# Optimization experiments

Hardware: AMD Instinct MI355X
Metric: run time of the kernel (lower is better)

The kernel has to match this reference:

```python
import jax, jax.numpy as jnp
import numpy as np

ZERO = 1e-8
L = 2            # num_gnn_layers
D = 256          # dim_node_features
B = 32           # graphs per batch
NPG = 256        # nodes per graph
N = B * NPG      # total nodes
E = 131072       # edges per edge-type
MAX_TOKENS = 256 # MAX_TOKENS_OF_A_POST
UPD = 0.5        # args.updated_weights_for_A


def _make_edges(k):
    k1, k2, k3 = jax.random.split(k, 3)
    g = jax.random.randint(k1, (E,), 0, B) * NPG          # keep edges within a graph
    src = g + jax.random.randint(k2, (E,), 0, NPG)
    dst = g + jax.random.randint(k3, (E,), 0, NPG)
    return jnp.stack([src, dst]).astype(jnp.int64)


def setup_inputs() -> dict:
    key = jax.random.key(0)
    ks = jax.random.split(key, 12)
    x = jax.random.normal(ks[0], (N, D), dtype=jnp.float32)
    ei_e = _make_edges(ks[1]); ew_e = jax.random.uniform(ks[2], (E,), dtype=jnp.float32)
    ei_p = _make_edges(ks[3]); ew_p = jax.random.uniform(ks[4], (E,), dtype=jnp.float32)
    ei_o = _make_edges(ks[5]); ew_o = jax.random.uniform(ks[6], (E,), dtype=jnp.float32)
    entity_mask = jax.random.randint(ks[7], (B, NPG), 0, 2).astype(bool)
    pattern_mask = jax.random.randint(ks[8], (B, NPG), 0, 2).astype(bool)
    s = 1.0 / np.sqrt(D)
    W_gcn = (jax.random.normal(ks[9], (L, 3, D, D), dtype=jnp.float32) * s)
    b_gcn = jnp.zeros((L, 3, D), dtype=jnp.float32)
    T_dyn = (jax.random.normal(ks[10], (L, D, D), dtype=jnp.float32) * s)
    return {
        'x': x,
        'edge_index_entity': ei_e, 'edge_weight_entity': ew_e,
        'edge_index_pattern': ei_p, 'edge_weight_pattern': ew_p,
        'edge_index_others': ei_o, 'edge_weight_others': ew_o,
        'entity_mask': entity_mask, 'pattern_mask': pattern_mask,
        'W_gcn': W_gcn, 'b_gcn': b_gcn, 'T_dyn': T_dyn,
    }


def _normalized_correlation_matrix(H):
    # cosine-similarity correlation matrix, symmetrically degree-normalized
    nrm = jnp.sqrt(jnp.sum(H * H, axis=1))
    A = (H @ H.T) / (nrm[:, None] * nrm[None, :] + ZERO)
    dinv = 1.0 / jnp.sqrt(jnp.abs(jnp.sum(A, axis=1)) + ZERO)
    return dinv[:, None] * A * dinv[None, :]


def _gcn(H, W, b, ei, ew):
    # GCNConv(add_self_loops=False, normalize=False): scatter-sum of weighted source messages
    msg = (H @ W)[ei[0]] * ew[:, None]                     # [E, D]
    return jax.ops.segment_sum(msg, ei[1], num_segments=N) + b


def _forward(x, we0, wp0, wo0, W_gcn, b_gcn, T_dyn,
             ei_e, ei_p, ei_o, entity_mask, pattern_mask):
    H = x
    A = _normalized_correlation_matrix(H)                  # [N, N]
    for i in range(L):
        if i == 0:
            we, wp, wo = we0, wp0, wo0
        else:
            # diag(one_hot(src) @ A @ one_hot(dst).T) == A[src, dst]
            we = A[ei_e[0], ei_e[1]]
            wp = A[ei_p[0], ei_p[1]]
            wo = A[ei_o[0], ei_o[1]]
        He = _gcn(H, W_gcn[i, 0], b_gcn[i, 0], ei_e, we)
        Hp = _gcn(H, W_gcn[i, 1], b_gcn[i, 1], ei_p, wp)
        Ho = _gcn(H, W_gcn[i, 2], b_gcn[i, 2], ei_o, wo)
        H = jax.nn.relu(He + Hp + Ho)
        A_hat = jax.nn.sigmoid((H @ T_dyn[i]) @ H.T)
        A = (1.0 - UPD) * A + UPD * A_hat
    # per-graph diagonal blocks of A  -> [B, NPG, NPG]
    A4 = A.reshape(B, NPG, B, NPG)
    idx = jnp.arange(B)
    blocks = A4[idx, :, idx, :]
    A_sum = jnp.sum(blocks, axis=-1)                       # [B, NPG]
    ent_cols = jnp.einsum('bij,bj->bi', blocks, entity_mask.astype(A.dtype))
    pat_cols = jnp.einsum('bij,bj->bi', blocks, pattern_mask.astype(A.dtype))
    map_pattern = A_sum - ent_cols
    map_entity = A_sum - pat_cols

    def finish(m):
        mn = jnp.min(m, axis=1, keepdims=True)
        mx = jnp.max(m, axis=1, keepdims=True)
        m = (m - mn) / (mx - mn + ZERO)
        m = m / (jnp.sum(m, axis=1, keepdims=True) + ZERO)
        return m[:, :MAX_TOKENS]                           # padding() with NPG==MAX_TOKENS

    return finish(map_entity), finish(map_pattern)


def reference(x, edge_index_entity, edge_weight_entity,
              edge_index_pattern, edge_weight_pattern,
              edge_index_others, edge_weight_others,
              entity_mask, pattern_mask, W_gcn, b_gcn, T_dyn):
    return _forward(x, edge_weight_entity, edge_weight_pattern, edge_weight_others,
                    W_gcn, b_gcn, T_dyn,
                    edge_index_entity, edge_index_pattern, edge_index_others,
                    entity_mask, pattern_mask)
```

## Files before the change

### kernel.cpp

```cpp
#include <hip/hip_runtime.h>

#define NND   8192
#define DDIM  256
#define NGRP  32
#define ZEROF 1e-8f
#define KSTR  72
#define TSTR  72
#define CCAP 192
#define SM_HALF 36864
#define SM_FULL 55296

typedef unsigned short u16;
typedef __attribute__((ext_vector_type(8))) short short8v;
typedef __attribute__((ext_vector_type(4))) float float4v;

__device__ inline u16 f2bf(float x) {
  unsigned u = __float_as_uint(x);
  u += 0x7fffu + ((u >> 16) & 1u);
  return (u16)(u >> 16);
}
__device__ inline float bf2f(u16 h) { return __uint_as_float((unsigned)h << 16); }
__device__ inline void split2(float x, u16& h, u16& l) {
  h = f2bf(x);
  l = f2bf(x - bf2f(h));
}

__device__ inline float wave_sum(float v) {
#pragma unroll
  for (int off = 32; off > 0; off >>= 1) v += __shfl_down(v, off, 64);
  return v;
}

#define LOAD_REGS(tt, kk)                                                                   \
  {                                                                                         \
    int m_ = tid >> 2, kq_ = (tid & 3) * 8;                                                 \
    size_t aoff_;                                                                           \
    if (MODE == 1)                                                                          \
      aoff_ = (size_t)((tt) * 256 + bym * 64 + m_) * 8192 + (size_t)(g * 256 + (kk) + kq_); \
    else if (MODE == 2 || MODE == 3 || MODE == 5)                                           \
      aoff_ = (size_t)(g * 256 + bym * 64 + m_) * 256 + (kk) + kq_;                         \
    else                                                                                    \
      aoff_ = (size_t)(bym * 64 + m_) * 256 + (kk) + kq_;                                   \
    rA[0][0] = *(const short8v*)&Ah_g[aoff_];                                               \
    rA[0][1] = *(const short8v*)&Ah_g[aoff_ + 32];                                          \
    rA[1][0] = *(const short8v*)&Al_g[aoff_];                                               \
    rA[1][1] = *(const short8v*)&Al_g[aoff_ + 32];                                          \
    size_t bbase_ = (MODE == 1) ? ((size_t)(g * 3 + (tt)) << 16)                            \
                  : ((MODE == 2 || MODE == 3 || MODE == 5) ? ((size_t)g << 16) : (size_t)0);\
    if (HALF) {                                                                             \
      int n_ = tid & 63, kq2_ = (tid >> 6) * 8;                                             \
      size_t boff_ = bbase_ + (size_t)(col0 + n_) * 256 + (kk) + kq2_;                      \
      rB[0][0] = *(const short8v*)&Bh_g[boff_];                                             \
      rB[0][1] = *(const short8v*)&Bh_g[boff_ + 32];                                        \
      rB[1][0] = *(const short8v*)&Bl_g[boff_];                                             \
      rB[1][1] = *(const short8v*)&Bl_g[boff_ + 32];                                        \
    } else {                                                                                \
      int n_ = tid & 127, kq2_ = (tid >> 7) * 16;                                           \
      size_t boff_ = bbase_ + (size_t)(col0 + n_) * 256 + (kk) + kq2_;                      \
      rB[0][0] = *(const short8v*)&Bh_g[boff_];     rB[0][1] = *(const short8v*)&Bh_g[boff_ + 8];  \
      rB[0][2] = *(const short8v*)&Bh_g[boff_ + 32]; rB[0][3] = *(const short8v*)&Bh_g[boff_ + 40];\
      rB[1][0] = *(const short8v*)&Bl_g[boff_];     rB[1][1] = *(const short8v*)&Bl_g[boff_ + 8];  \
      rB[1][2] = *(const short8v*)&Bl_g[boff_ + 32]; rB[1][3] = *(const short8v*)&Bl_g[boff_ + 40];\
    }                                                                                       \
  }

template<int MODE, bool HALF>
__device__ __forceinline__ void mfma_body(
    u16* lds,
    const u16* __restrict__ Ah_g, const u16* __restrict__ Al_g,
    const u16* __restrict__ Bh_g, const u16* __restrict__ Bl_g,
    float* __restrict__ Cf, u16* __restrict__ Ch, u16* __restrict__ Cl,
    const float* __restrict__ nrm, const float* __restrict__ dinv,
    const float* __restrict__ bias,
    int bxm, int bym, int g) {
  u16* Ahs = lds;
  u16* Als = lds + 4608;
  u16* Bhs = lds + 9216;
  u16* Bls = lds + 9216 + (HALF ? 4608 : 9216);
  u16* Tt  = lds + 9216;
  const int NJ = HALF ? 2 : 4;
  const int tid = threadIdx.x;
  const int col0 = bxm * (HALF ? 64 : 128);
  const int w = tid >> 6, lane = tid & 63;
  const int lm = lane & 15, lq = lane >> 4;
  const int wr = (w >> 1) * 32, wc = (w & 1) * (HALF ? 32 : 64);

  float4v acc[2][4];
#pragma unroll
  for (int i = 0; i < 2; ++i)
#pragma unroll
    for (int j = 0; j < NJ; ++j) acc[i][j] = (float4v)0.f;

  short8v rA[2][2], rB[2][4];
  const int TOTAL = (MODE == 1) ? 12 : 4;

  LOAD_REGS(0, 0);
  for (int step = 0; step < TOTAL; ++step) {
    if (step) __syncthreads();
    {
      int m = tid >> 2, kq = (tid & 3) * 8;
      *(short8v*)&Ahs[m * KSTR + kq]      = rA[0][0];
      *(short8v*)&Ahs[m * KSTR + kq + 32] = rA[0][1];
      *(short8v*)&Als[m * KSTR + kq]      = rA[1][0];
      *(short8v*)&Als[m * KSTR + kq + 32] = rA[1][1];
    }
    if (HALF) {
      int n = tid & 63, kq2 = (tid >> 6) * 8;
      *(short8v*)&Bhs[n * KSTR + kq2]      = rB[0][0];
      *(short8v*)&Bhs[n * KSTR + kq2 + 32] = rB[0][1];
      *(short8v*)&Bls[n * KSTR + kq2]      = rB[1][0];
      *(short8v*)&Bls[n * KSTR + kq2 + 32] = rB[1][1];
    } else {
      int n = tid & 127, kq2 = (tid >> 7) * 16;
      *(short8v*)&Bhs[n * KSTR + kq2]      = rB[0][0];
      *(short8v*)&Bhs[n * KSTR + kq2 + 8]  = rB[0][1];
      *(short8v*)&Bhs[n * KSTR + kq2 + 32] = rB[0][2];
      *(short8v*)&Bhs[n * KSTR + kq2 + 40] = rB[0][3];
      *(short8v*)&Bls[n * KSTR + kq2]      = rB[1][0];
      *(short8v*)&Bls[n * KSTR + kq2 + 8]  = rB[1][1];
      *(short8v*)&Bls[n * KSTR + kq2 + 32] = rB[1][2];
      *(short8v*)&Bls[n * KSTR + kq2 + 40] = rB[1][3];
    }
    __syncthreads();
    int nxt = step + 1;
    if (nxt < TOTAL) {
      if (MODE == 1) { LOAD_REGS(nxt >> 2, (nxt & 3) * 64); }
      else           { LOAD_REGS(0, nxt * 64); }
    }
#pragma unroll
    for (int sub = 0; sub < 2; ++sub) {
      const int co = sub * 32 + lq * 8;
      short8v ah[2], al[2], bh[4], bl[4];
#pragma unroll
      for (int i = 0; i < 2; ++i) {
        int r = wr + i * 16 + lm;
        ah[i] = *(const short8v*)&Ahs[r * KSTR + co];
        al[i] = *(const short8v*)&Als[r * KSTR + co];
      }
#pragma unroll
      for (int j = 0; j < NJ; ++j) {
        int r = wc + j * 16 + lm;
        bh[j] = *(const short8v*)&Bhs[r * KSTR + co];
        bl[j] = *(const short8v*)&Bls[r * KSTR + co];
      }
#pragma unroll
      for (int i = 0; i < 2; ++i)
#pragma unroll
        for (int j = 0; j < NJ; ++j) {
          acc[i][j] = __builtin_amdgcn_mfma_f32_16x16x32_bf16(ah[i], bh[j], acc[i][j], 0, 0, 0);
          acc[i][j] = __builtin_amdgcn_mfma_f32_16x16x32_bf16(ah[i], bl[j], acc[i][j], 0, 0, 0);
          acc[i][j] = __builtin_amdgcn_mfma_f32_16x16x32_bf16(al[i], bh[j], acc[i][j], 0, 0, 0);
        }
    }
  }

  if (MODE == 2 || MODE == 3 || MODE == 5) {
#pragma unroll
    for (int i = 0; i < 2; ++i) {
#pragma unroll
      for (int r = 0; r < 4; ++r) {
        int grow = g * 256 + bym * 64 + wr + i * 16 + lq * 4 + r;
        float di = 0.f, ni = 0.f;
        if (MODE == 5) { di = dinv[grow]; ni = nrm[grow]; }
#pragma unroll
        for (int j = 0; j < NJ; ++j) {
          int gcol = col0 + wc + j * 16 + lm;
          size_t ci = (size_t)grow * 256 + gcol;
          float v = acc[i][j][r];
          if (MODE == 2) {
            Cf[ci] = v;
          } else if (MODE == 3) {
            Cf[ci] = 0.5f * Cf[ci] + 0.5f * (1.f / (1.f + expf(-v)));
          } else {
            int gj = g * 256 + gcol;
            float scale = di * dinv[gj] / (ni * nrm[gj] + ZEROF);
            Cf[ci] = 0.5f * Cf[ci] * scale + 0.5f * (1.f / (1.f + expf(-v)));
          }
        }
      }
    }
  } else {
    float bsum[8];
    if (MODE == 1) {
#pragma unroll
      for (int i = 0; i < 2; ++i)
#pragma unroll
        for (int r = 0; r < 4; ++r) {
          int d = bym * 64 + wr + i * 16 + lq * 4 + r;
          bsum[i * 4 + r] = bias[d] + bias[256 + d] + bias[512 + d];
        }
    }
    u16 hv[32], lv[32];
#pragma unroll
    for (int i = 0; i < 2; ++i)
#pragma unroll
      for (int j = 0; j < NJ; ++j)
#pragma unroll
        for (int r = 0; r < 4; ++r) {
          float v = acc[i][j][r];
          if (MODE == 1) v = fmaxf(v + bsum[i * 4 + r], 0.f);
          split2(v, hv[(i * 4 + r) * NJ + j], lv[(i * 4 + r) * NJ + j]);
        }
    int ebase1 = (MODE == 1) ? (g * 256 + col0) : col0;
    int ebase2 = bym * 64;
    size_t estride = (MODE == 0) ? 8192 : 256;
#pragma unroll
    for (int ph = 0; ph < 2; ++ph) {
      __syncthreads();
      const u16* sv = ph ? lv : hv;
#pragma unroll
      for (int i = 0; i < 2; ++i)
#pragma unroll
        for (int j = 0; j < NJ; ++j)
#pragma unroll
          for (int r = 0; r < 4; ++r)
            Tt[(wc + j * 16 + lm) * TSTR + wr + i * 16 + lq * 4 + r] = sv[(i * 4 + r) * NJ + j];
      __syncthreads();
      u16* dst = ph ? Cl : Ch;
      int cc0 = tid >> 3, mm0 = (tid & 7) * 8;
#pragma unroll
      for (int it = 0; it < (HALF ? 2 : 4); ++it) {
        int cc = it * 32 + cc0;
        short8v v = *(const short8v*)&Tt[cc * TSTR + mm0];
        *(short8v*)&dst[(size_t)(ebase1 + cc) * estride + ebase2 + mm0] = v;
      }
    }
  }
}

__device__ __forceinline__ void mbuild_body(
    float* tile, int bid, int l,
    const uint2* __restrict__ recs2, const int* __restrict__ bcnt2,
    const float* __restrict__ Abuf, u16* __restrict__ Mbh, u16* __restrict__ Mbl) {
  const int tid = threadIdx.x;
  int gt = bid >> 3, chunk = bid & 7;
  int g = gt / 3;
  float4 z = make_float4(0.f, 0.f, 0.f, 0.f);
#pragma unroll
  for (int k = 0; k < 8; ++k) ((float4*)tile)[k * 256 + tid] = z;
  __syncthreads();
#pragma unroll
  for (int c = 0; c < 8; ++c) {
    int cnt = bcnt2[bid * 8 + c];
    const uint2* rp = &recs2[(size_t)bid * (8 * CCAP) + (size_t)c * CCAP];
    for (int k = tid; k < cnt; k += 256) {
      uint2 r = rp[k];
      int s = r.x & 255, d5 = (r.x >> 8) & 31;
      float w = l ? Abuf[(size_t)(g * 256 + s) * 256 + chunk * 32 + d5]
                  : __uint_as_float(r.y);
      atomicAdd(&tile[d5 * 256 + s], w);
    }
  }
  __syncthreads();
  size_t base4 = ((size_t)gt << 14) + ((size_t)chunk << 11);
#pragma unroll
  for (int k = 0; k < 8; ++k) {
    float4 f = ((float4*)tile)[k * 256 + tid];
    ushort4 h, lo;
    split2(f.x, h.x, lo.x); split2(f.y, h.y, lo.y);
    split2(f.z, h.z, lo.z); split2(f.w, h.w, lo.w);
    ((ushort4*)Mbh)[base4 + k * 256 + tid] = h;
    ((ushort4*)Mbl)[base4 + k * 256 + tid] = lo;
  }
}

__global__ void k_prep(const int* __restrict__ e0, const int* __restrict__ e1,
                       const int* __restrict__ e2, const unsigned char* __restrict__ m0,
                       const unsigned char* __restrict__ m1,
                       const float* __restrict__ W, const float* __restrict__ T,
                       const float* __restrict__ x,
                       const float* __restrict__ ew0, const float* __restrict__ ew1,
                       const float* __restrict__ ew2,
                       float* __restrict__ emf, float* __restrict__ pmf,
                       u16* __restrict__ Wth, u16* __restrict__ Wtl,
                       u16* __restrict__ sct, uint2* __restrict__ recs,
                       float* __restrict__ nrm, float* __restrict__ Spart,
                       u16* __restrict__ Hh, u16* __restrict__ Hl,
                       int E_, int nCvt, int nBkt) {
  __shared__ float tile[32][33];
  __shared__ float inv[64];
  __shared__ int nz[1];
  __shared__ unsigned int hcnt[768];
  __shared__ unsigned int hoff[768];
  __shared__ unsigned int ppart[256];
  __shared__ uint2 stage[768];
  const int b = blockIdx.x, tid = threadIdx.x;
  if (b < nCvt) {
    if (tid == 0) nz[0] = 0;
    __syncthreads();
    int i4 = tid * 4;
    int c = (m0[i4 + 1] != 0) + (m0[i4 + 2] != 0) + (m0[i4 + 3] != 0);
    if (c) atomicAdd(&nz[0], c);
    __syncthreads();
    int fM = (nz[0] == 0);
    int i = b * 256 + tid;
    if (i < NND) {
      unsigned char v = fM ? m0[4 * i] : m0[i];
      emf[i] = 1.f - (float)(v != 0);
    } else {
      int j = i - NND;
      unsigned char v = fM ? m1[4 * j] : m1[j];
      pmf[j] = 1.f - (float)(v != 0);
    }
  } else if (b < nCvt + nBkt) {
    if (tid == 0) nz[0] = 0;
    hcnt[tid] = 0; hcnt[tid + 256] = 0; hcnt[tid + 512] = 0;
    __syncthreads();
    if (e0[2 * tid + 1] != 0) atomicAdd(&nz[0], 1);
    __syncthreads();
    int fE = (nz[0] == 0);
    int e = (b - nCvt) * 256 + tid;
    bool valid = (e < E_);
    int mybid[3]; unsigned int myrec[3]; float myw[3];
    if (valid) {
#pragma unroll
      for (int t = 0; t < 3; ++t) {
        const int* ei = (t == 0) ? e0 : ((t == 1) ? e1 : e2);
        int src = fE ? ei[2 * e] : ei[e];
        int dst = fE ? ei[2 * (E_ + e)] : ei[E_ + e];
        int g = src >> 8, s = src & 255, d = dst & 255;
        mybid[t] = ((g * 3 + t) << 3) | (d >> 5);
        myrec[t] = (unsigned)(((d & 31) << 8) | s);
        myw[t] = (t == 0 ? ew0 : (t == 1 ? ew1 : ew2))[e];
        atomicAdd(&hcnt[mybid[t]], 1u);
      }
    }
    __syncthreads();
    unsigned c0 = hcnt[3 * tid], c1 = hcnt[3 * tid + 1], c2 = hcnt[3 * tid + 2];
    unsigned tsum = c0 + c1 + c2;
    ppart[tid] = tsum;
    __syncthreads();
    for (int off = 1; off < 256; off <<= 1) {
      unsigned v = (tid >= off) ? ppart[tid - off] : 0u;
      __syncthreads();
      ppart[tid] += v;
      __syncthreads();
    }
    unsigned base = ppart[tid] - tsum;
    hoff[3 * tid] = base;
    hoff[3 * tid + 1] = base + c0;
    hoff[3 * tid + 2] = base + c0 + c1;
    __syncthreads();
#pragma unroll
    for (int k = 0; k < 3; ++k) {
      int bin = tid + k * 256;
      unsigned cc = hcnt[bin]; if (cc > 31u) cc = 31u;
      sct[(size_t)(b - nCvt) * 768 + bin] = (u16)(hoff[bin] | (cc << 11));
    }
    __syncthreads();
    if (valid) {
#pragma unroll
      for (int t = 0; t < 3; ++t) {
        unsigned slot = atomicAdd(&hoff[mybid[t]], 1u);
        stage[slot] = make_uint2(myrec[t], __float_as_uint(myw[t]));
      }
    }
    __syncthreads();
    uint2* dstp = &recs[(size_t)(b - nCvt) * 768];
    dstp[tid] = stage[tid];
    dstp[tid + 256] = stage[tid + 256];
    dstp[tid + 512] = stage[tid + 512];
  } else if (b < nCvt + nBkt + 512) {
    int bb = b - nCvt - nBkt;
    int mat = bb >> 6, rem = bb & 63;
    int k0 = (rem >> 3) * 32, n0 = (rem & 7) * 32;
    const float* src = (mat < 6) ? (W + (size_t)mat * 65536) : (T + (size_t)(mat - 6) * 65536);
    int r = tid >> 3, c4 = (tid & 7) * 4;
    const float4 v = *(const float4*)&src[(size_t)(k0 + r) * 256 + n0 + c4];
    tile[r][c4 + 0] = v.x; tile[r][c4 + 1] = v.y; tile[r][c4 + 2] = v.z; tile[r][c4 + 3] = v.w;
    __syncthreads();
    float o[4] = {tile[c4 + 0][r], tile[c4 + 1][r], tile[c4 + 2][r], tile[c4 + 3][r]};
    u16 hh[4], ll[4];
#pragma unroll
    for (int q = 0; q < 4; ++q) split2(o[q], hh[q], ll[q]);
    size_t off = (size_t)mat * 65536 + (size_t)(n0 + r) * 256 + k0 + c4;
    *(ushort4*)&Wth[off] = *(ushort4*)hh;
    *(ushort4*)&Wtl[off] = *(ushort4*)ll;
  } else {
    int bn = b - nCvt - nBkt - 512;
    int n0 = bn * 64;
    int w = tid >> 6, lane = tid & 63;
    for (int it = 0; it < 16; ++it) {
      int nl = it * 4 + w;
      int node = n0 + nl;
      const float4 v = *(const float4*)&x[(size_t)node * 256 + lane * 4];
      u16 hh[4], ll[4];
      split2(v.x, hh[0], ll[0]); split2(v.y, hh[1], ll[1]);
      split2(v.z, hh[2], ll[2]); split2(v.w, hh[3], ll[3]);
      *(ushort4*)&Hh[(size_t)node * 256 + lane * 4] = *(ushort4*)hh;
      *(ushort4*)&Hl[(size_t)node * 256 + lane * 4] = *(ushort4*)ll;
      float s = wave_sum(v.x * v.x + v.y * v.y + v.z * v.z + v.w * v.w);
      if (lane == 0) { float nr = sqrtf(s); nrm[node] = nr; inv[nl] = 1.f / nr; }
    }
    __syncthreads();
    float s = 0.f;
    for (int i = 0; i < 64; ++i) s += x[(size_t)(n0 + i) * 256 + tid] * inv[i];
    Spart[bn * 256 + tid] = s;
  }
}

__global__ void k_reorder(const u16* __restrict__ sct, const uint2* __restrict__ recs,
                          uint2* __restrict__ recs2, int* __restrict__ bcnt2, int nBkt) {
  const int wid = blockIdx.x * 4 + (threadIdx.x >> 6);
  const int lane = threadIdx.x & 63;
  const int bid = wid >> 3;
  const int c = wid & 7;
  const int nseg = nBkt >> 3;
  unsigned cnt = 0, start = 0;
  int bb = c * nseg + lane;
  if (lane < nseg) {
    unsigned sc = sct[(size_t)bb * 768 + bid];
    start = sc & 2047u; cnt = sc >> 11;
  }
  unsigned pre = cnt;
#pragma unroll
  for (int off = 1; off < 64; off <<= 1) {
    unsigned v = __shfl_up(pre, off, 64);
    if (lane >= off) pre += v;
  }
  unsigned excl = pre - cnt;
  unsigned total = __shfl(pre, 63, 64);
  uint2* dst = &recs2[(size_t)bid * (8 * CCAP) + (size_t)c * CCAP];
  const uint2* rp = &recs[(size_t)bb * 768 + start];
  for (unsigned k = 0; k < cnt; ++k) {
    unsigned o = excl + k;
    if (o < CCAP) dst[o] = rp[k];
  }
  if (lane == 0) bcnt2[bid * 8 + c] = (total > CCAP) ? CCAP : total;
}

__global__ __launch_bounds__(256, 2) void k_stageA(
    const u16* __restrict__ Hinh, const u16* __restrict__ Hinl,
    const u16* __restrict__ Wth, const u16* __restrict__ Wtl,
    u16* __restrict__ XWTh, u16* __restrict__ XWTl,
    const uint2* __restrict__ recs2, const int* __restrict__ bcnt2,
    u16* __restrict__ Mbh, u16* __restrict__ Mbl,
    float* __restrict__ Abuf,
    const float* __restrict__ x, const float* __restrict__ Spart,
    const float* __restrict__ nrm, float* __restrict__ dinv) {
  extern __shared__ u16 lds[];
  const int b = blockIdx.x;
  if (b < 768) {
    mfma_body<0, false>(lds, Hinh, Hinl, Wth, Wtl,
                        nullptr, XWTh, XWTl, nullptr, nullptr, nullptr,
                        b >> 7, b & 127, 0);
  } else if (b < 1536) {
    mbuild_body((float*)lds, b - 768, 0, recs2, bcnt2, nullptr, Mbh, Mbl);
  } else if (b < 2048) {
    int bb = b - 1536;
    int g = bb & 31, r = bb >> 5;
    mfma_body<2, true>(lds, Hinh, Hinl, Hinh, Hinl, Abuf, nullptr, nullptr,
                       nullptr, nullptr, nullptr, r >> 2, r & 3, g);
  } else {
    float* Sl = (float*)lds;
    const int tid = threadIdx.x;
    float s = 0.f;
    for (int bb = 0; bb < 128; ++bb) s += Spart[bb * 256 + tid];
    Sl[tid] = s;
    __syncthreads();
    int base = (b - 2048) * 64;
    int w = tid >> 6, lane = tid & 63;
    const float4 sv = *(const float4*)&Sl[lane * 4];
    for (int it = 0; it < 16; ++it) {
      int node = base + it * 4 + w;
      const float4 v = *(const float4*)&x[(size_t)node * 256 + lane * 4];
      float s2 = wave_sum(v.x * sv.x + v.y * sv.y + v.z * sv.z + v.w * sv.w);
      if (lane == 0) {
        float rowsum = s2 / nrm[node];
        dinv[node] = rsqrtf(fabsf(rowsum) + ZEROF);
      }
    }
  }
}

__global__ __launch_bounds__(256, 2) void k_stageA2(
    const u16* __restrict__ H2h, const u16* __restrict__ H2l,
    const u16* __restrict__ Wth, const u16* __restrict__ Wtl,
    u16* __restrict__ XWTh, u16* __restrict__ XWTl,
    const uint2* __restrict__ recs2, const int* __restrict__ bcnt2,
    const float* __restrict__ Abuf,
    u16* __restrict__ Mbh, u16* __restrict__ Mbl) {
  extern __shared__ u16 lds[];
  const int b = blockIdx.x;
  if (b < 768) {
    mfma_body<0, false>(lds, H2h, H2l, Wth + (size_t)768 * 256, Wtl + (size_t)768 * 256,
                        nullptr, XWTh, XWTl, nullptr, nullptr, nullptr,
                        b >> 7, b & 127, 0);
  } else {
    mbuild_body((float*)lds, b - 768, 1, recs2, bcnt2, Abuf, Mbh, Mbl);
  }
}

__global__ __launch_bounds__(256, 2) void k_stageB(
    const u16* __restrict__ XWTh, const u16* __restrict__ XWTl,
    const u16* __restrict__ Mbh, const u16* __restrict__ Mbl,
    u16* __restrict__ Houth, u16* __restrict__ Houtl, const float* __restrict__ bias) {
  extern __shared__ u16 lds[];
  const int b = blockIdx.x;
  int g = b & 31, r = b >> 5;
  mfma_body<1, true>(lds, XWTh, XWTl, Mbh, Mbl,
                     nullptr, Houth, Houtl, nullptr, nullptr, bias,
                     r >> 2, r & 3, g);
}

__global__ __launch_bounds__(256, 2) void k_stageC(
    const u16* __restrict__ Wth, const u16* __restrict__ Wtl, int l,
    const u16* __restrict__ Hh, const u16* __restrict__ Hl,
    u16* __restrict__ tmph, u16* __restrict__ tmpl) {
  extern __shared__ u16 lds[];
  const int b = blockIdx.x;
  mfma_body<4, true>(lds, Wth + (size_t)(6 + l) * 65536, Wtl + (size_t)(6 + l) * 65536,
                     Hh, Hl, nullptr, tmph, tmpl, nullptr, nullptr, nullptr,
                     b & 127, b >> 7, 0);
}

__global__ __launch_bounds__(256, 2) void k_stageD(
    const u16* __restrict__ tmph, const u16* __restrict__ tmpl,
    const u16* __restrict__ Hh, const u16* __restrict__ Hl,
    float* __restrict__ Abuf,
    const float* __restrict__ nrm, const float* __restrict__ dinv, int scaled) {
  extern __shared__ u16 lds[];
  const int b = blockIdx.x;
  int g = b & 31, r = b >> 5;
  if (scaled)
    mfma_body<5, true>(lds, tmph, tmpl, Hh, Hl, Abuf, nullptr, nullptr,
                       nrm, dinv, nullptr, r >> 2, r & 3, g);
  else
    mfma_body<3, true>(lds, tmph, tmpl, Hh, Hl, Abuf, nullptr, nullptr,
                       nullptr, nullptr, nullptr, r >> 2, r & 3, g);
}

__global__ void k_maps(const float* __restrict__ Abuf, const float* __restrict__ emf,
                       const float* __restrict__ pmf, float* __restrict__ out) {
  __shared__ float sme[256], smp[256], red[256];
  const int g = blockIdx.x, tid = threadIdx.x, w = tid >> 6, lane = tid & 63;
  const int j0 = g * 256 + lane * 4;
  const float4 pmv = *(const float4*)&pmf[j0];
  const float4 emv = *(const float4*)&emf[j0];
  for (int it = 0; it < 64; ++it) {
    int nl = it * 4 + w;
    const float4 a = *(const float4*)&Abuf[((size_t)g * 256 + nl) * 256 + lane * 4];
    float me = a.x * pmv.x + a.y * pmv.y + a.z * pmv.z + a.w * pmv.w;
    float mp = a.x * emv.x + a.y * emv.y + a.z * emv.z + a.w * emv.w;
#pragma unroll
    for (int off = 32; off > 0; off >>= 1) {
      me += __shfl_down(me, off, 64);
      mp += __shfl_down(mp, off, 64);
    }
    if (lane == 0) { sme[nl] = me; smp[nl] = mp; }
  }
  __syncthreads();
  for (int which = 0; which < 2; ++which) {
    float v = which ? smp[tid] : sme[tid];
    red[tid] = v; __syncthreads();
    for (int s = 128; s > 0; s >>= 1) { if (tid < s) red[tid] = fminf(red[tid], red[tid + s]); __syncthreads(); }
    float mn = red[0]; __syncthreads();
    red[tid] = v; __syncthreads();
    for (int s = 128; s > 0; s >>= 1) { if (tid < s) red[tid] = fmaxf(red[tid], red[tid + s]); __syncthreads(); }
    float mx = red[0]; __syncthreads();
    float m = (v - mn) / (mx - mn + ZEROF);
    red[tid] = m; __syncthreads();
    for (int s = 128; s > 0; s >>= 1) { if (tid < s) red[tid] += red[tid + s]; __syncthreads(); }
    float sum = red[0]; __syncthreads();
    out[which * NND + g * 256 + tid] = m / (sum + ZEROF);
  }
}

extern "C" void kernel_launch(void* const* d_in, const int* in_sizes, int n_in,
                              void* d_out, int out_size, void* d_ws, size_t ws_size,
                              hipStream_t stream) {
  const float* x = (const float*)d_in[0];
  const unsigned char* em_raw = (const unsigned char*)d_in[7];
  const unsigned char* pm_raw = (const unsigned char*)d_in[8];
  const float* W  = (const float*)d_in[9];
  const float* bg = (const float*)d_in[10];
  const float* T  = (const float*)d_in[11];
  float* out = (float*)d_out;
  const int E_ = in_sizes[2];

  const int nCvt = (2 * NND) / 256;
  const int nBkt = (E_ + 255) / 256;

  float* ws = (float*)d_ws;
  size_t o = 0;
  float* Abuf = ws + o; o += (size_t)NND * 256;
  u16* Mbh_l0 = (u16*)(ws + o); o += (size_t)NGRP * 3 * 65536 / 2;
  u16* Mbl_l0 = (u16*)(ws + o); o += (size_t)NGRP * 3 * 65536 / 2;
  u16* Mbh_l1 = (u16*)(ws + o); o += (size_t)NGRP * 3 * 65536 / 2;
  u16* Mbl_l1 = (u16*)(ws + o); o += (size_t)NGRP * 3 * 65536 / 2;
  u16* Hh   = (u16*)(ws + o); o += (size_t)NND * 256 / 2;
  u16* Hl   = (u16*)(ws + o); o += (size_t)NND * 256 / 2;
  u16* H2h  = (u16*)(ws + o); o += (size_t)NND * 256 / 2;
  u16* H2l  = (u16*)(ws + o); o += (size_t)NND * 256 / 2;
  u16* tmph = (u16*)(ws + o); o += (size_t)NND * 256 / 2;
  u16* tmpl = (u16*)(ws + o); o += (size_t)NND * 256 / 2;
  u16* XWTh = (u16*)(ws + o); o += (size_t)768 * NND / 2;
  u16* XWTl = (u16*)(ws + o); o += (size_t)768 * NND / 2;
  u16* Wth  = (u16*)(ws + o); o += (size_t)8 * 65536 / 2;
  u16* Wtl  = (u16*)(ws + o); o += (size_t)8 * 65536 / 2;
  float* nrm   = ws + o; o += NND;
  float* dinv  = ws + o; o += NND;
  float* Spart = ws + o; o += 128 * 256;
  float* emf   = ws + o; o += NND;
  float* pmf   = ws + o; o += NND;
  u16* sct     = (u16*)(ws + o); o += (size_t)nBkt * 768 / 2;
  uint2* recs  = (uint2*)(ws + o); o += (size_t)nBkt * 768 * 2;
  uint2* recs2 = (uint2*)(ws + o); o += (size_t)768 * 8 * CCAP * 2;
  int* bcnt2   = (int*)(ws + o); o += (size_t)768 * 8;

  const float* ew0 = (const float*)d_in[2];
  const float* ew1 = (const float*)d_in[4];
  const float* ew2 = (const float*)d_in[6];

  k_prep<<<nCvt + nBkt + 512 + 128, 256, 0, stream>>>(
      (const int*)d_in[1], (const int*)d_in[3], (const int*)d_in[5], em_raw, pm_raw,
      W, T, x, ew0, ew1, ew2, emf, pmf, Wth, Wtl, sct, recs,
      nrm, Spart, Hh, Hl, E_, nCvt, nBkt);

  k_reorder<<<1536, 256, 0, stream>>>(sct, recs, recs2, bcnt2, nBkt);

  k_stageA<<<2176, 256, SM_FULL, stream>>>(Hh, Hl, Wth, Wtl, XWTh, XWTl,
                                           recs2, bcnt2, Mbh_l0, Mbl_l0, Abuf,
                                           x, Spart, nrm, dinv);
  k_stageB<<<512, 256, SM_HALF, stream>>>(XWTh, XWTl, Mbh_l0, Mbl_l0, H2h, H2l, bg);
  k_stageC<<<512, 256, SM_HALF, stream>>>(Wth, Wtl, 0, H2h, H2l, tmph, tmpl);
  k_stageD<<<512, 256, SM_HALF, stream>>>(tmph, tmpl, H2h, H2l, Abuf, nrm, dinv, 1);

  k_stageA2<<<1536, 256, SM_FULL, stream>>>(H2h, H2l, Wth, Wtl, XWTh, XWTl,
                                            recs2, bcnt2, Abuf, Mbh_l1, Mbl_l1);
  k_stageB<<<512, 256, SM_HALF, stream>>>(XWTh, XWTl, Mbh_l1, Mbl_l1, Hh, Hl, bg + 768);
  k_stageC<<<512, 256, SM_HALF, stream>>>(Wth, Wtl, 1, Hh, Hl, tmph, tmpl);
  k_stageD<<<512, 256, SM_HALF, stream>>>(tmph, tmpl, Hh, Hl, Abuf, nullptr, nullptr, 0);

  k_maps<<<NGRP, 256, 0, stream>>>(Abuf, emf, pmf, out);
}
```

Measured before the change: 283.1 us.

## Double-buffer GEMM tiles with direct global-to-LDS loads and XOR swizzle

Replaces the register-staged global→LDS copy with direct global_load_lds 16-byte transfers into a double-buffered LDS layout, so the next K-slice streams in while MFMAs run on the current one. K-step shrinks from 64 to 32 and padded strides are replaced by an XOR swizzle to avoid bank conflicts, which lowers LDS use. This removes one barrier per step and the register round-trip, at the cost of twice as many loop iterations and reliance on the direct-to-LDS load path and its synchronisation being correct.

```diff
diff --git a/kernel.cpp b/kernel.cpp
--- a/kernel.cpp
+++ b/kernel.cpp
@@ -4,15 +4,20 @@
 #define DDIM  256
 #define NGRP  32
 #define ZEROF 1e-8f
-#define KSTR  72
 #define TSTR  72
 #define CCAP 192
-#define SM_HALF 36864
-#define SM_FULL 55296
+#define SM_HALF 32768
+#define SM_FULL 49152
 
 typedef unsigned short u16;
 typedef __attribute__((ext_vector_type(8))) short short8v;
 typedef __attribute__((ext_vector_type(4))) float float4v;
+
+__device__ __forceinline__ void gl16(const u16* g, u16* l) {
+  __builtin_amdgcn_global_load_lds(
+      (const __attribute__((address_space(1))) unsigned int*)g,
+      (__attribute__((address_space(3))) unsigned int*)l, 16, 0, 0);
+}
 
 __device__ inline u16 f2bf(float x) {
   unsigned u = __float_as_uint(x);
@@ -30,39 +35,6 @@
   for (int off = 32; off > 0; off >>= 1) v += __shfl_down(v, off, 64);
   return v;
 }
-
-#define LOAD_REGS(tt, kk)                                                                   \
-  {                                                                                         \
-    int m_ = tid >> 2, kq_ = (tid & 3) * 8;                                                 \
-    size_t aoff_;                                                                           \
-    if (MODE == 1)                                                                          \
-      aoff_ = (size_t)((tt) * 256 + bym * 64 + m_) * 8192 + (size_t)(g * 256 + (kk) + kq_); \
-    else if (MODE == 2 || MODE == 3 || MODE == 5)                                           \
-      aoff_ = (size_t)(g * 256 + bym * 64 + m_) * 256 + (kk) + kq_;                         \
-    else                                                                                    \
-      aoff_ = (size_t)(bym * 64 + m_) * 256 + (kk) + kq_;                                   \
-    rA[0][0] = *(const short8v*)&Ah_g[aoff_];                                               \
-    rA[0][1] = *(const short8v*)&Ah_g[aoff_ + 32];                                          \
-    rA[1][0] = *(const short8v*)&Al_g[aoff_];                                               \
-    rA[1][1] = *(const short8v*)&Al_g[aoff_ + 32];                                          \
-    size_t bbase_ = (MODE == 1) ? ((size_t)(g * 3 + (tt)) << 16)                            \
-                  : ((MODE == 2 || MODE == 3 || MODE == 5) ? ((size_t)g << 16) : (size_t)0);\
-    if (HALF) {                                                                             \
-      int n_ = tid & 63, kq2_ = (tid >> 6) * 8;                                             \
-      size_t boff_ = bbase_ + (size_t)(col0 + n_) * 256 + (kk) + kq2_;                      \
-      rB[0][0] = *(const short8v*)&Bh_g[boff_];                                             \
-      rB[0][1] = *(const short8v*)&Bh_g[boff_ + 32];                                        \
-      rB[1][0] = *(const short8v*)&Bl_g[boff_];                                             \
-      rB[1][1] = *(const short8v*)&Bl_g[boff_ + 32];                                        \
-    } else {                                                                                \
-      int n_ = tid & 127, kq2_ = (tid >> 7) * 16;                                           \
-      size_t boff_ = bbase_ + (size_t)(col0 + n_) * 256 + (kk) + kq2_;                      \
-      rB[0][0] = *(const short8v*)&Bh_g[boff_];     rB[0][1] = *(const short8v*)&Bh_g[boff_ + 8];  \
-      rB[0][2] = *(const short8v*)&Bh_g[boff_ + 32]; rB[0][3] = *(const short8v*)&Bh_g[boff_ + 40];\
-      rB[1][0] = *(const short8v*)&Bl_g[boff_];     rB[1][1] = *(const short8v*)&Bl_g[boff_ + 8];  \
-      rB[1][2] = *(const short8v*)&Bl_g[boff_ + 32]; rB[1][3] = *(const short8v*)&Bl_g[boff_ + 40];\
-    }                                                                                       \
-  }
 
 template<int MODE, bool HALF>
 __device__ __forceinline__ void mfma_body(
@@ -73,17 +45,20 @@
     const float* __restrict__ nrm, const float* __restrict__ dinv,
     const float* __restrict__ bias,
     int bxm, int bym, int g) {
-  u16* Ahs = lds;
-  u16* Als = lds + 4608;
-  u16* Bhs = lds + 9216;
-  u16* Bls = lds + 9216 + (HALF ? 4608 : 9216);
-  u16* Tt  = lds + 9216;
+  const int BS    = HALF ? 8192 : 12288;
+  const int BOFF  = 4096;
+  const int BLOFF = 4096 + (HALF ? 2048 : 4096);
   const int NJ = HALF ? 2 : 4;
   const int tid = threadIdx.x;
   const int col0 = bxm * (HALF ? 64 : 128);
   const int w = tid >> 6, lane = tid & 63;
   const int lm = lane & 15, lq = lane >> 4;
   const int wr = (w >> 1) * 32, wc = (w & 1) * (HALF ? 32 : 64);
+  const int TOTAL = (MODE == 1) ? 24 : 8;
+
+  const int m_ = tid >> 2;
+  const int sw = ((tid & 3) ^ (m_ & 3)) * 8;
+  const int wbase = (tid >> 6) * 512;
 
   float4v acc[2][4];
 #pragma unroll
@@ -91,69 +66,68 @@
 #pragma unroll
     for (int j = 0; j < NJ; ++j) acc[i][j] = (float4v)0.f;
 
-  short8v rA[2][2], rB[2][4];
-  const int TOTAL = (MODE == 1) ? 12 : 4;
-
-  LOAD_REGS(0, 0);
+  auto STAGE = [&](int buf, int tt, int kk) {
+    u16* base = lds + buf * BS;
+    size_t aoff;
+    if (MODE == 1)
+      aoff = (size_t)(tt * 256 + bym * 64 + m_) * 8192 + (size_t)(g * 256 + kk + sw);
+    else if (MODE == 2 || MODE == 3 || MODE == 5)
+      aoff = (size_t)(g * 256 + bym * 64 + m_) * 256 + kk + sw;
+    else
+      aoff = (size_t)(bym * 64 + m_) * 256 + kk + sw;
+    gl16(&Ah_g[aoff], base + wbase);
+    gl16(&Al_g[aoff], base + 2048 + wbase);
+    size_t bbase = (MODE == 1) ? ((size_t)(g * 3 + tt) << 16)
+                 : ((MODE == 2 || MODE == 3 || MODE == 5) ? ((size_t)g << 16) : (size_t)0);
+    size_t boff = bbase + (size_t)(col0 + m_) * 256 + kk + sw;
+    gl16(&Bh_g[boff], base + BOFF + wbase);
+    gl16(&Bl_g[boff], base + BLOFF + wbase);
+    if (!HALF) {
+      size_t boff2 = boff + (size_t)64 * 256;
+      gl16(&Bh_g[boff2], base + BOFF + 2048 + wbase);
+      gl16(&Bl_g[boff2], base + BLOFF + 2048 + wbase);
+    }
+  };
+
+  STAGE(0, 0, 0);
+  __syncthreads();
+  int cur = 0;
   for (int step = 0; step < TOTAL; ++step) {
-    if (step) __syncthreads();
-    {
-      int m = tid >> 2, kq = (tid & 3) * 8;
-      *(short8v*)&Ahs[m * KSTR + kq]      = rA[0][0];
-      *(short8v*)&Ahs[m * KSTR + kq + 32] = rA[0][1];
-      *(short8v*)&Als[m * KSTR + kq]      = rA[1][0];
-      *(short8v*)&Als[m * KSTR + kq + 32] = rA[1][1];
-    }
-    if (HALF) {
-      int n = tid & 63, kq2 = (tid >> 6) * 8;
-      *(short8v*)&Bhs[n * KSTR + kq2]      = rB[0][0];
-      *(short8v*)&Bhs[n * KSTR + kq2 + 32] = rB[0][1];
-      *(short8v*)&Bls[n * KSTR + kq2]      = rB[1][0];
-      *(short8v*)&Bls[n * KSTR + kq2 + 32] = rB[1][1];
-    } else {
-      int n = tid & 127, kq2 = (tid >> 7) * 16;
-      *(short8v*)&Bhs[n * KSTR + kq2]      = rB[0][0];
-      *(short8v*)&Bhs[n * KSTR + kq2 + 8]  = rB[0][1];
-      *(short8v*)&Bhs[n * KSTR + kq2 + 32] = rB[0][2];
-      *(short8v*)&Bhs[n * KSTR + kq2 + 40] = rB[0][3];
-      *(short8v*)&Bls[n * KSTR + kq2]      = rB[1][0];
-      *(short8v*)&Bls[n * KSTR + kq2 + 8]  = rB[1][1];
-      *(short8v*)&Bls[n * KSTR + kq2 + 32] = rB[1][2];
-      *(short8v*)&Bls[n * KSTR + kq2 + 40] = rB[1][3];
-    }
-    __syncthreads();
     int nxt = step + 1;
     if (nxt < TOTAL) {
-      if (MODE == 1) { LOAD_REGS(nxt >> 2, (nxt & 3) * 64); }
-      else           { LOAD_REGS(0, nxt * 64); }
-    }
-#pragma unroll
-    for (int sub = 0; sub < 2; ++sub) {
-      const int co = sub * 32 + lq * 8;
-      short8v ah[2], al[2], bh[4], bl[4];
-#pragma unroll
-      for (int i = 0; i < 2; ++i) {
-        int r = wr + i * 16 + lm;
-        ah[i] = *(const short8v*)&Ahs[r * KSTR + co];
-        al[i] = *(const short8v*)&Als[r * KSTR + co];
+      int tt = (MODE == 1) ? (nxt >> 3) : 0;
+      int kk = (MODE == 1) ? ((nxt & 7) * 32) : (nxt * 32);
+      STAGE(cur ^ 1, tt, kk);
+    }
+    u16* base = lds + cur * BS;
+    short8v ah[2], al[2], bh[4], bl[4];
+#pragma unroll
+    for (int i = 0; i < 2; ++i) {
+      int r = wr + i * 16 + lm;
+      int sa = (lq ^ (r & 3)) * 8;
+      ah[i] = *(const short8v*)&base[r * 32 + sa];
+      al[i] = *(const short8v*)&base[2048 + r * 32 + sa];
+    }
+#pragma unroll
+    for (int j = 0; j < NJ; ++j) {
+      int rb = wc + j * 16 + lm;
+      int sb = (lq ^ (rb & 3)) * 8;
+      bh[j] = *(const short8v*)&base[BOFF + rb * 32 + sb];
+      bl[j] = *(const short8v*)&base[BLOFF + rb * 32 + sb];
+    }
+#pragma unroll
+    for (int i = 0; i < 2; ++i)
+#pragma unroll
+      for (int j = 0; j < NJ; ++j) {
+        acc[i][j] = __builtin_amdgcn_mfma_f32_16x16x32_bf16(ah[i], bh[j], acc[i][j], 0, 0, 0);
+        acc[i][j] = __builtin_amdgcn_mfma_f32_16x16x32_bf16(ah[i], bl[j], acc[i][j], 0, 0, 0);
+        acc[i][j] = __builtin_amdgcn_mfma_f32_16x16x32_bf16(al[i], bh[j], acc[i][j], 0, 0, 0);
       }
-#pragma unroll
-      for (int j = 0; j < NJ; ++j) {
-        int r = wc + j * 16 + lm;
-        bh[j] = *(const short8v*)&Bhs[r * KSTR + co];
-        bl[j] = *(const short8v*)&Bls[r * KSTR + co];
-      }
-#pragma unroll
-      for (int i = 0; i < 2; ++i)
-#pragma unroll
-        for (int j = 0; j < NJ; ++j) {
-          acc[i][j] = __builtin_amdgcn_mfma_f32_16x16x32_bf16(ah[i], bh[j], acc[i][j], 0, 0, 0);
-          acc[i][j] = __builtin_amdgcn_mfma_f32_16x16x32_bf16(ah[i], bl[j], acc[i][j], 0, 0, 0);
-          acc[i][j] = __builtin_amdgcn_mfma_f32_16x16x32_bf16(al[i], bh[j], acc[i][j], 0, 0, 0);
-        }
-    }
-  }
-
+    __syncthreads();
+    cur ^= 1;
+  }
+
+  u16* Tt = lds;
   if (MODE == 2 || MODE == 3 || MODE == 5) {
 #pragma unroll
     for (int i = 0; i < 2; ++i) {
```

New measurement: 257.4 us. -9.1%, faster.
